# Kernel tuning notes

Hardware: AMD Instinct MI355X
Metric: run time of the kernel (lower is better)

Reference implementation:

```python
import jax, jax.numpy as jnp
import numpy as np

# Static point-cloud layout: B clouds of P points each (batch ids are contiguous equal-size segments)
B, P, C = 16, 4096, 64
RATIO, K = 0.25, 32
S = int(P * RATIO)  # 1024 sampled points per cloud
H1, H2, OUT = 64, 64, 128
CIN = C + 3


def _fps(pos):
    """Farthest point sampling on one cloud. pos: [P,3] -> idx [S] (start at point 0)."""
    Pn = pos.shape[0]
    def step(carry, _):
        dist, far = carry
        d = jnp.sum((pos - pos[far]) ** 2, axis=-1)   # sq dist to newest sample
        dist = jnp.minimum(dist, d)                    # dist to nearest selected point
        nxt = jnp.argmax(dist).astype(jnp.int32)
        return (dist, nxt), far
    init = (jnp.full((Pn,), jnp.inf, pos.dtype), jnp.int32(0))
    _, idx = jax.lax.scan(step, init, None, length=S)
    return idx


def _gather(a, i):
    # a: [B, P, ...], i: [B, ...int] -> per-batch fancy gather
    return jax.vmap(lambda ab, ib: ab[ib])(a, i)


def setup_inputs() -> dict:
    key = jax.random.key(0)
    ks = jax.random.split(key, 6)
    N = B * P
    x = jax.random.normal(ks[0], (N, C), jnp.float32)
    pos = jax.random.uniform(ks[1], (N, 3), jnp.float32)  # points in unit cube
    batch = jnp.repeat(jnp.arange(B, dtype=jnp.int32), P)
    W1 = jax.random.normal(ks[2], (CIN, H1), jnp.float32) / np.float32(np.sqrt(CIN))
    b1 = jnp.zeros((H1,), jnp.float32)
    W2 = jax.random.normal(ks[3], (H1, H2), jnp.float32) / np.float32(np.sqrt(H1))
    b2 = jnp.zeros((H2,), jnp.float32)
    W3 = jax.random.normal(ks[4], (H2, OUT), jnp.float32) / np.float32(np.sqrt(H2))
    b3 = jnp.zeros((OUT,), jnp.float32)
    return {"x": x, "pos": pos, "batch": batch,
            "W1": W1, "b1": b1, "W2": W2, "b2": b2, "W3": W3, "b3": b3}


def reference(x, pos, batch, W1, b1, W2, b2, W3, b3):
    xb = x.reshape(B, P, C)
    pb = pos.reshape(B, P, 3)
    bb = batch.reshape(B, P)

    # 1) FPS sampling per cloud
    idx = jax.vmap(_fps)(pb)                                   # [B,S]
    pos_q = _gather(pb, idx)                                   # [B,S,3]

    # 2) kNN grouping: k nearest original points for each sampled point
    d2 = jnp.sum((pos_q[:, :, None, :] - pb[:, None, :, :]) ** 2, axis=-1)  # [B,S,P]
    _, nbr = jax.lax.top_k(-d2, K)                             # [B,S,K]

    # 3) PointNetConv: MLP(concat[x_j, pos_j - pos_i]) then max-aggregate over neighbors
    x_j = _gather(xb, nbr)                                     # [B,S,K,C]
    p_j = _gather(pb, nbr)                                     # [B,S,K,3]
    rel = p_j - pos_q[:, :, None, :]
    h = jnp.concatenate([x_j, rel], axis=-1)                   # [B,S,K,C+3]
    h = jax.nn.relu(h @ W1 + b1)
    h = jax.nn.relu(h @ W2 + b2)
    h = h @ W3 + b3                                            # plain last layer (PyG MLP plain_last)
    out = jnp.max(h, axis=2)                                   # [B,S,OUT]  max aggr

    batch_q = _gather(bb, idx)                                 # [B,S]
    return out.reshape(B * S, OUT), pos_q.reshape(B * S, 3), batch_q.reshape(B * S)
```

## Files before the change

kernel.cpp:

```cpp
#include <hip/hip_runtime.h>
#include <math.h>
#include <string.h>

#define NB   16
#define NP   4096
#define NC   64
#define NS   1024
#define NK   32
#define NH1  64
#define NH2  64
#define NOUT 128

typedef unsigned long long u64;
typedef unsigned int u32;
typedef unsigned short u16;
typedef __attribute__((ext_vector_type(8))) short s16x8;
typedef __attribute__((ext_vector_type(4))) float f32x4;

__device__ inline u64 umin64(u64 a, u64 b) { return a < b ? a : b; }
__device__ inline u64 umax64(u64 a, u64 b) { return a > b ? a : b; }

__device__ inline u16 f2bf(float f) {
  u32 x = __float_as_uint(f);
  return (u16)((x + 0x7fffu + ((x >> 16) & 1u)) >> 16);
}
__device__ inline u32 pack2bf(float a, float b) {
  return (u32)f2bf(a) | ((u32)f2bf(b) << 16);
}

__device__ inline float d2exact(float ax, float ay, float az,
                                float qx, float qy, float qz) {
  float dx = __fsub_rn(ax, qx), dy = __fsub_rn(ay, qy), dz = __fsub_rn(az, qz);
  return __fadd_rn(__fadd_rn(__fmul_rn(dx, dx), __fmul_rn(dy, dy)),
                   __fmul_rn(dz, dz));
}

#define DPP_LVL_MAX(CTRL)                                                     \
  {                                                                           \
    u32 lo = (u32)key, hi = (u32)(key >> 32);                                 \
    u32 plo = (u32)__builtin_amdgcn_update_dpp((int)lo, (int)lo, CTRL, 0xF, 0xF, false); \
    u32 phi = (u32)__builtin_amdgcn_update_dpp((int)hi, (int)hi, CTRL, 0xF, 0xF, false); \
    u64 ok = ((u64)phi << 32) | plo;                                          \
    key = (ok > key) ? ok : key;                                              \
  }
__device__ inline u64 dpp_wavemax_u64(u64 key) {
  DPP_LVL_MAX(0x111) DPP_LVL_MAX(0x112) DPP_LVL_MAX(0x114)
  DPP_LVL_MAX(0x118) DPP_LVL_MAX(0x142) DPP_LVL_MAX(0x143)
  return key;
}
#define DPP_LVL_MIN(CTRL)                                                     \
  {                                                                           \
    u32 lo = (u32)key, hi = (u32)(key >> 32);                                 \
    u32 plo = (u32)__builtin_amdgcn_update_dpp((int)lo, (int)lo, CTRL, 0xF, 0xF, false); \
    u32 phi = (u32)__builtin_amdgcn_update_dpp((int)hi, (int)hi, CTRL, 0xF, 0xF, false); \
    u64 ok = ((u64)phi << 32) | plo;                                          \
    key = (ok < key) ? ok : key;                                              \
  }
__device__ inline u64 dpp_wavemin_bcast_u64(u64 key) {
  DPP_LVL_MIN(0x111) DPP_LVL_MIN(0x112) DPP_LVL_MIN(0x114)
  DPP_LVL_MIN(0x118) DPP_LVL_MIN(0x142) DPP_LVL_MIN(0x143)
  u32 lo = (u32)__builtin_amdgcn_readlane((int)(u32)key, 63);
  u32 hi = (u32)__builtin_amdgcn_readlane((int)(u32)(key >> 32), 63);
  return ((u64)hi << 32) | lo;
}

#define DPP_FMAX_STAGE(CTRL)                                                  \
  do {                                                                        \
    _Pragma("unroll")                                                         \
    for (int mt = 0; mt < 8; ++mt) {                                          \
      _Pragma("unroll")                                                       \
      for (int r = 0; r < 4; ++r) {                                           \
        int vi = __float_as_int(m[mt][r]);                                    \
        int ov = __builtin_amdgcn_update_dpp(vi, vi, CTRL, 0xF, 0xF, false);  \
        m[mt][r] = fmaxf(m[mt][r], __int_as_float(ov));                       \
      }                                                                       \
    }                                                                         \
  } while (0)

__global__ __launch_bounds__(256) void fps_kernel(const float* __restrict__ pos,
                                                  float* __restrict__ pos_q,
                                                  float* __restrict__ batch_q) {
  const int b = blockIdx.x;
  const int tid = threadIdx.x;
  const int wave = tid >> 6;
  const float* pb = pos + (size_t)b * NP * 3;

  __shared__ float lx[NP], ly[NP], lz[NP];
  __shared__ u64 s_key[2][4];
  __shared__ int s_idx[NS];

  float px[16], py[16], pz[16], dist[16];
#pragma unroll
  for (int i = 0; i < 16; ++i) {
    int p = i * 256 + tid;
    float xx = pb[p * 3 + 0];
    float yy = pb[p * 3 + 1];
    float zz = pb[p * 3 + 2];
    px[i] = xx; py[i] = yy; pz[i] = zz;
    lx[p] = xx; ly[p] = yy; lz[p] = zz;
    dist[i] = __builtin_inff();
  }
  __syncthreads();

  float fx = lx[0], fy = ly[0], fz = lz[0];
  int far = 0;

  for (int s = 0; s < NS; ++s) {
    if (tid == 0) s_idx[s] = far;

    float bv = -1.0f; int bp = 0;
#pragma unroll
    for (int i = 0; i < 16; ++i) {
      float dx = __fsub_rn(px[i], fx);
      float dy = __fsub_rn(py[i], fy);
      float dz = __fsub_rn(pz[i], fz);
      float d = __fadd_rn(__fadd_rn(__fmul_rn(dx, dx), __fmul_rn(dy, dy)),
                          __fmul_rn(dz, dz));
      d = fminf(dist[i], d);
      dist[i] = d;
      if (d > bv) { bv = d; bp = i * 256 + tid; }
    }

    u64 key = ((u64)__float_as_uint(bv) << 32) | (u32)(NP - 1 - bp);
    key = dpp_wavemax_u64(key);
    if ((tid & 63) == 63) s_key[s & 1][wave] = key;
    __syncthreads();

    u64 k0 = s_key[s & 1][0];
    u64 k1 = s_key[s & 1][1];
    u64 k2 = s_key[s & 1][2];
    u64 k3 = s_key[s & 1][3];
    u64 km = umax64(umax64(k0, k1), umax64(k2, k3));
    far = NP - 1 - (int)(u32)(km & 0xFFFFFFFFull);
    fx = lx[far]; fy = ly[far]; fz = lz[far];
  }
  __syncthreads();

  for (int s = tid; s < NS; s += 256) {
    int p = s_idx[s];
    size_t o = (size_t)(b * NS + s);
    pos_q[o * 3 + 0] = lx[p];
    pos_q[o * 3 + 1] = ly[p];
    pos_q[o * 3 + 2] = lz[p];
    batch_q[o] = (float)b;
  }
}

__device__ inline void ins4(u64& b0, u64& b1, u64& b2, u64& b3, u64 k) {
  u64 m0 = umax64(b0, k); b0 = umin64(b0, k);
  u64 m1 = umax64(b1, m0); b1 = umin64(b1, m0);
  u64 m2 = umax64(b2, m1); b2 = umin64(b2, m1);
  b3 = umin64(b3, m2);
}

__global__ __launch_bounds__(64) void knn_kernel(const float* __restrict__ pos,
                                                 const float* __restrict__ pos_q,
                                                 int* __restrict__ nbr) {
  const u64 KMAX = ~0ull;
  const int q = blockIdx.x;
  const int b = q >> 10;
  const int lane = threadIdx.x;
  const float* pb = pos + (size_t)b * NP * 3;
  const float qx = pos_q[q * 3 + 0];
  const float qy = pos_q[q * 3 + 1];
  const float qz = pos_q[q * 3 + 2];

  u64 b0 = KMAX, b1 = KMAX, b2 = KMAX, b3 = KMAX;
#pragma unroll 4
  for (int gg = 0; gg < 16; ++gg) {
    int p = gg * 256 + lane * 4;
    const float* s = pb + (size_t)p * 3;
    float4 v0 = *(const float4*)(s);
    float4 v1 = *(const float4*)(s + 4);
    float4 v2 = *(const float4*)(s + 8);
    float d0 = d2exact(v0.x, v0.y, v0.z, qx, qy, qz);
    float d1 = d2exact(v0.w, v1.x, v1.y, qx, qy, qz);
    float d2 = d2exact(v1.z, v1.w, v2.x, qx, qy, qz);
    float d3 = d2exact(v2.y, v2.z, v2.w, qx, qy, qz);
    ins4(b0, b1, b2, b3, ((u64)__float_as_uint(d0) << 32) | (u32)(p + 0));
    ins4(b0, b1, b2, b3, ((u64)__float_as_uint(d1) << 32) | (u32)(p + 1));
    ins4(b0, b1, b2, b3, ((u64)__float_as_uint(d2) << 32) | (u32)(p + 2));
    ins4(b0, b1, b2, b3, ((u64)__float_as_uint(d3) << 32) | (u32)(p + 3));
  }

  u64 exmask = 0ull;
  for (int r = 0; r < NK; ++r) {
    u64 kmin = dpp_wavemin_bcast_u64(b0);
    u32 p = (u32)kmin;
    if (lane == 0) nbr[q * NK + r] = (int)p;
    if (((p >> 2) & 63u) == (u32)lane) {
      b0 = b1; b1 = b2; b2 = b3; b3 = KMAX;
      exmask |= 1ull << (((p >> 8) << 2) | (p & 3u));
      if (b0 == KMAX) {
        for (int gg = 0; gg < 16; ++gg) {
          int pp = gg * 256 + lane * 4;
          const float* s = pb + (size_t)pp * 3;
          float4 v0 = *(const float4*)(s);
          float4 v1 = *(const float4*)(s + 4);
          float4 v2 = *(const float4*)(s + 8);
          float dd[4];
          dd[0] = d2exact(v0.x, v0.y, v0.z, qx, qy, qz);
          dd[1] = d2exact(v0.w, v1.x, v1.y, qx, qy, qz);
          dd[2] = d2exact(v1.z, v1.w, v2.x, qx, qy, qz);
          dd[3] = d2exact(v2.y, v2.z, v2.w, qx, qy, qz);
#pragma unroll
          for (int rr = 0; rr < 4; ++rr) {
            int slot = gg * 4 + rr;
            if ((exmask >> slot) & 1ull) continue;
            ins4(b0, b1, b2, b3,
                 ((u64)__float_as_uint(dd[rr]) << 32) | (u32)(pp + rr));
          }
        }
      }
    }
  }
}

#define WF_L2 6144
#define WF_L3 10240
#define WF_TOT 18432

__global__ __launch_bounds__(256) void prep_kernel(
    const float* __restrict__ W1, const float* __restrict__ W2,
    const float* __restrict__ W3, u16* __restrict__ wf) {
  int flat = blockIdx.x * 256 + threadIdx.x;
  if (flat >= WF_TOT) return;
  float val;
  int j = flat & 7, lane = (flat >> 3) & 63, t = flat >> 9;
  int k8 = 8 * (lane >> 4) + j, li = lane & 15;
  if (flat < WF_L2) {
    int kc = t % 3, mt = t / 3;
    int k = kc * 32 + k8;
    val = (k < 67) ? W1[k * 64 + mt * 16 + li] : 0.0f;
  } else if (flat < WF_L3) {
    t -= WF_L2 >> 9;
    int kc = t & 1, mt = t >> 1;
    val = W2[(kc * 32 + k8) * 64 + mt * 16 + li];
  } else {
    t -= WF_L3 >> 9;
    int kc = t & 1, mt = t >> 1;
    val = W3[(kc * 32 + k8) * 128 + mt * 16 + li];
  }
  wf[flat] = f2bf(val);
}

#define HST 72

__global__ __launch_bounds__(256) void conv_kernel(
    const float* __restrict__ x, const float* __restrict__ pos,
    const u16* __restrict__ wf,
    const float* __restrict__ b1, const float* __restrict__ b2,
    const float* __restrict__ b3,
    const int* __restrict__ nbr, const float* __restrict__ pos_q,
    float* __restrict__ out) {
  __shared__ u16 Hs[4][32][HST];

  const int tid = threadIdx.x, wave = tid >> 6, lane = tid & 63;
  const int q = blockIdx.x * 4 + wave;
  const int b = q >> 10;
  const int g = lane >> 4, li = lane & 15;

  const int n0 = nbr[q * NK + li];
  const int n1 = nbr[q * NK + li + 16];
  const float qx = pos_q[q * 3 + 0];
  const float qy = pos_q[q * 3 + 1];
  const float qz = pos_q[q * 3 + 2];

  uint4 bf1[2][3];
  {
    const float* xb = x + (size_t)b * NP * NC;
#pragma unroll
    for (int nt = 0; nt < 2; ++nt) {
      const float* s = xb + (size_t)(nt ? n1 : n0) * NC + 8 * g;
#pragma unroll
      for (int kc = 0; kc < 2; ++kc) {
        float4 v0 = *(const float4*)(s + kc * 32);
        float4 v1 = *(const float4*)(s + kc * 32 + 4);
        bf1[nt][kc] = make_uint4(pack2bf(v0.x, v0.y), pack2bf(v0.z, v0.w),
                                 pack2bf(v1.x, v1.y), pack2bf(v1.z, v1.w));
      }
      const float* pp = pos + ((size_t)b * NP + (nt ? n1 : n0)) * 3;
      float rx = __fsub_rn(pp[0], qx);
      float ry = __fsub_rn(pp[1], qy);
      float rz = __fsub_rn(pp[2], qz);
      uint4 w = make_uint4(0u, 0u, 0u, 0u);
      if (g == 0) { w.x = pack2bf(rx, ry); w.y = pack2bf(rz, 0.0f); }
      bf1[nt][2] = w;
    }
  }

  const uint4* wf4 = (const uint4*)wf;

  {
    f32x4 acc[4][2];
#pragma unroll
    for (int mt = 0; mt < 4; ++mt) {
      float4 bb = *(const float4*)(b1 + mt * 16 + 4 * g);
      acc[mt][0] = f32x4{bb.x, bb.y, bb.z, bb.w};
      acc[mt][1] = acc[mt][0];
    }
#pragma unroll
    for (int mt = 0; mt < 4; ++mt)
#pragma unroll
      for (int kc = 0; kc < 3; ++kc) {
        uint4 aw = wf4[(mt * 3 + kc) * 64 + lane];
        s16x8 a = __builtin_bit_cast(s16x8, aw);
        acc[mt][0] = __builtin_amdgcn_mfma_f32_16x16x32_bf16(
            a, __builtin_bit_cast(s16x8, bf1[0][kc]), acc[mt][0], 0, 0, 0);
        acc[mt][1] = __builtin_amdgcn_mfma_f32_16x16x32_bf16(
            a, __builtin_bit_cast(s16x8, bf1[1][kc]), acc[mt][1], 0, 0, 0);
      }
#pragma unroll
    for (int mt = 0; mt < 4; ++mt)
#pragma unroll
      for (int nt = 0; nt < 2; ++nt) {
        f32x4 v = acc[mt][nt];
        u32 w0 = pack2bf(fmaxf(v[0], 0.f), fmaxf(v[1], 0.f));
        u32 w1 = pack2bf(fmaxf(v[2], 0.f), fmaxf(v[3], 0.f));
        *(uint2*)&Hs[wave][li + 16 * nt][mt * 16 + 4 * g] = make_uint2(w0, w1);
      }
  }
  asm volatile("s_waitcnt lgkmcnt(0)" ::: "memory");

  {
    uint4 bf2[2][2];
#pragma unroll
    for (int nt = 0; nt < 2; ++nt)
#pragma unroll
      for (int kc = 0; kc < 2; ++kc)
        bf2[nt][kc] = *(const uint4*)&Hs[wave][li + 16 * nt][kc * 32 + 8 * g];

    f32x4 acc[4][2];
#pragma unroll
    for (int mt = 0; mt < 4; ++mt) {
      float4 bb = *(const float4*)(b2 + mt * 16 + 4 * g);
      acc[mt][0] = f32x4{bb.x, bb.y, bb.z, bb.w};
      acc[mt][1] = acc[mt][0];
    }
#pragma unroll
    for (int mt = 0; mt < 4; ++mt)
#pragma unroll
      for (int kc = 0; kc < 2; ++kc) {
        uint4 aw = wf4[(WF_L2 >> 3) + (mt * 2 + kc) * 64 + lane];
        s16x8 a = __builtin_bit_cast(s16x8, aw);
        acc[mt][0] = __builtin_amdgcn_mfma_f32_16x16x32_bf16(
            a, __builtin_bit_cast(s16x8, bf2[0][kc]), acc[mt][0], 0, 0, 0);
        acc[mt][1] = __builtin_amdgcn_mfma_f32_16x16x32_bf16(
            a, __builtin_bit_cast(s16x8, bf2[1][kc]), acc[mt][1], 0, 0, 0);
      }
#pragma unroll
    for (int mt = 0; mt < 4; ++mt)
#pragma unroll
      for (int nt = 0; nt < 2; ++nt) {
        f32x4 v = acc[mt][nt];
        u32 w0 = pack2bf(fmaxf(v[0], 0.f), fmaxf(v[1], 0.f));
        u32 w1 = pack2bf(fmaxf(v[2], 0.f), fmaxf(v[3], 0.f));
        *(uint2*)&Hs[wave][li + 16 * nt][mt * 16 + 4 * g] = make_uint2(w0, w1);
      }
  }
  asm volatile("s_waitcnt lgkmcnt(0)" ::: "memory");

  {
    uint4 bf3[2][2];
#pragma unroll
    for (int nt = 0; nt < 2; ++nt)
#pragma unroll
      for (int kc = 0; kc < 2; ++kc)
        bf3[nt][kc] = *(const uint4*)&Hs[wave][li + 16 * nt][kc * 32 + 8 * g];

    f32x4 acc[8][2];
#pragma unroll
    for (int mt = 0; mt < 8; ++mt) {
      float4 bb = *(const float4*)(b3 + mt * 16 + 4 * g);
      acc[mt][0] = f32x4{bb.x, bb.y, bb.z, bb.w};
      acc[mt][1] = acc[mt][0];
    }
#pragma unroll
    for (int mt = 0; mt < 8; ++mt)
#pragma unroll
      for (int kc = 0; kc < 2; ++kc) {
        uint4 aw = wf4[(WF_L3 >> 3) + (mt * 2 + kc) * 64 + lane];
        s16x8 a = __builtin_bit_cast(s16x8, aw);
        acc[mt][0] = __builtin_amdgcn_mfma_f32_16x16x32_bf16(
            a, __builtin_bit_cast(s16x8, bf3[0][kc]), acc[mt][0], 0, 0, 0);
        acc[mt][1] = __builtin_amdgcn_mfma_f32_16x16x32_bf16(
            a, __builtin_bit_cast(s16x8, bf3[1][kc]), acc[mt][1], 0, 0, 0);
      }

    float m[8][4];
#pragma unroll
    for (int mt = 0; mt < 8; ++mt)
#pragma unroll
      for (int r = 0; r < 4; ++r)
        m[mt][r] = fmaxf(acc[mt][0][r], acc[mt][1][r]);

    DPP_FMAX_STAGE(0xB1);
    DPP_FMAX_STAGE(0x4E);
    DPP_FMAX_STAGE(0x141);
    DPP_FMAX_STAGE(0x140);

#pragma unroll
    for (int mt = 0; mt < 8; ++mt) {
      if (li == mt) {
        float4 o = make_float4(m[mt][0], m[mt][1], m[mt][2], m[mt][3]);
        *(float4*)(out + (size_t)q * NOUT + mt * 16 + 4 * g) = o;
      }
    }
  }
}

extern "C" void kernel_launch(void* const* d_in, const int* in_sizes, int n_in,
                              void* d_out, int out_size, void* d_ws, size_t ws_size,
                              hipStream_t stream) {
  (void)in_sizes; (void)n_in; (void)out_size; (void)ws_size;
  const float* x   = (const float*)d_in[0];
  const float* pos = (const float*)d_in[1];
  const float* W1 = (const float*)d_in[3];
  const float* b1 = (const float*)d_in[4];
  const float* W2 = (const float*)d_in[5];
  const float* b2 = (const float*)d_in[6];
  const float* W3 = (const float*)d_in[7];
  const float* b3 = (const float*)d_in[8];

  float* out     = (float*)d_out;
  float* pos_q   = out + (size_t)NB * NS * NOUT;
  float* batch_q = pos_q + (size_t)NB * NS * 3;

  int* nbr = (int*)d_ws;
  u16* wfrag = (u16*)((char*)d_ws + (size_t)NB * NS * NK * 4);

  hipLaunchKernelGGL(prep_kernel, dim3((WF_TOT + 255) / 256), dim3(256), 0,
                     stream, W1, W2, W3, wfrag);
  hipLaunchKernelGGL(fps_kernel, dim3(NB), dim3(256), 0, stream,
                     pos, pos_q, batch_q);
  hipLaunchKernelGGL(knn_kernel, dim3(NB * NS), dim3(64), 0, stream,
                     pos, pos_q, nbr);
  hipLaunchKernelGGL(conv_kernel, dim3(NB * NS / 4), dim3(256), 0, stream,
                     x, pos, wfrag, b1, b2, b3, nbr, pos_q, out);
}
```

Before: 781.1 us.

## Fuse FPS, kNN and conv into one cooperative persistent kernel with progress flags

Merges the FPS, kNN and PointNet conv kernels into a single cooperative launch. Sixteen blocks run FPS and publish sampled positions plus a per-cloud progress counter with release stores. The remaining blocks pull query indices from an atomic work queue, spin until their sample is published, then run kNN and the MLP in registers without writing neighbour indices to global memory. This overlaps the serial FPS phase with the kNN/conv work and removes the nbr round-trip and separate launches, at the cost of spin-waiting, a fixed grid of 256 blocks at one block per CU, and dependence on the work queue ordering to avoid deadlock.

New measurement: 1.148 ms. +47.0%, slower.

```diff
diff --git a/kernel.cpp b/kernel.cpp
--- a/kernel.cpp
+++ b/kernel.cpp
@@ -1,15 +1,13 @@
 #include <hip/hip_runtime.h>
 #include <math.h>
-#include <string.h>
 
 #define NB   16
 #define NP   4096
 #define NC   64
 #define NS   1024
 #define NK   32
-#define NH1  64
-#define NH2  64
 #define NOUT 128
+#define NQ   (NB * NS)
 
 typedef unsigned long long u64;
 typedef unsigned int u32;
@@ -77,75 +75,6 @@
     }                                                                         \
   } while (0)
 
-__global__ __launch_bounds__(256) void fps_kernel(const float* __restrict__ pos,
-                                                  float* __restrict__ pos_q,
-                                                  float* __restrict__ batch_q) {
-  const int b = blockIdx.x;
-  const int tid = threadIdx.x;
-  const int wave = tid >> 6;
-  const float* pb = pos + (size_t)b * NP * 3;
-
-  __shared__ float lx[NP], ly[NP], lz[NP];
-  __shared__ u64 s_key[2][4];
-  __shared__ int s_idx[NS];
-
-  float px[16], py[16], pz[16], dist[16];
-#pragma unroll
-  for (int i = 0; i < 16; ++i) {
-    int p = i * 256 + tid;
-    float xx = pb[p * 3 + 0];
-    float yy = pb[p * 3 + 1];
-    float zz = pb[p * 3 + 2];
-    px[i] = xx; py[i] = yy; pz[i] = zz;
-    lx[p] = xx; ly[p] = yy; lz[p] = zz;
-    dist[i] = __builtin_inff();
-  }
-  __syncthreads();
-
-  float fx = lx[0], fy = ly[0], fz = lz[0];
-  int far = 0;
-
-  for (int s = 0; s < NS; ++s) {
-    if (tid == 0) s_idx[s] = far;
-
-    float bv = -1.0f; int bp = 0;
-#pragma unroll
-    for (int i = 0; i < 16; ++i) {
-      float dx = __fsub_rn(px[i], fx);
-      float dy = __fsub_rn(py[i], fy);
-      float dz = __fsub_rn(pz[i], fz);
-      float d = __fadd_rn(__fadd_rn(__fmul_rn(dx, dx), __fmul_rn(dy, dy)),
-                          __fmul_rn(dz, dz));
-      d = fminf(dist[i], d);
-      dist[i] = d;
-      if (d > bv) { bv = d; bp = i * 256 + tid; }
-    }
-
-    u64 key = ((u64)__float_as_uint(bv) << 32) | (u32)(NP - 1 - bp);
-    key = dpp_wavemax_u64(key);
-    if ((tid & 63) == 63) s_key[s & 1][wave] = key;
-    __syncthreads();
-
-    u64 k0 = s_key[s & 1][0];
-    u64 k1 = s_key[s & 1][1];
-    u64 k2 = s_key[s & 1][2];
-    u64 k3 = s_key[s & 1][3];
-    u64 km = umax64(umax64(k0, k1), umax64(k2, k3));
-    far = NP - 1 - (int)(u32)(km & 0xFFFFFFFFull);
-    fx = lx[far]; fy = ly[far]; fz = lz[far];
-  }
-  __syncthreads();
-
-  for (int s = tid; s < NS; s += 256) {
-    int p = s_idx[s];
-    size_t o = (size_t)(b * NS + s);
-    pos_q[o * 3 + 0] = lx[p];
-    pos_q[o * 3 + 1] = ly[p];
-    pos_q[o * 3 + 2] = lz[p];
-    batch_q[o] = (float)b;
-  }
-}
-
 __device__ inline void ins4(u64& b0, u64& b1, u64& b2, u64& b3, u64 k) {
   u64 m0 = umax64(b0, k); b0 = umin64(b0, k);
   u64 m1 = umax64(b1, m0); b1 = umin64(b1, m0);
@@ -153,76 +82,15 @@
   b3 = umin64(b3, m2);
 }
 
-__global__ __launch_bounds__(64) void knn_kernel(const float* __restrict__ pos,
-                                                 const float* __restrict__ pos_q,
-                                                 int* __restrict__ nbr) {
-  const u64 KMAX = ~0ull;
-  const int q = blockIdx.x;
-  const int b = q >> 10;
-  const int lane = threadIdx.x;
-  const float* pb = pos + (size_t)b * NP * 3;
-  const float qx = pos_q[q * 3 + 0];
-  const float qy = pos_q[q * 3 + 1];
-  const float qz = pos_q[q * 3 + 2];
-
-  u64 b0 = KMAX, b1 = KMAX, b2 = KMAX, b3 = KMAX;
-#pragma unroll 4
-  for (int gg = 0; gg < 16; ++gg) {
-    int p = gg * 256 + lane * 4;
-    const float* s = pb + (size_t)p * 3;
-    float4 v0 = *(const float4*)(s);
-    float4 v1 = *(const float4*)(s + 4);
-    float4 v2 = *(const float4*)(s + 8);
-    float d0 = d2exact(v0.x, v0.y, v0.z, qx, qy, qz);
-    float d1 = d2exact(v0.w, v1.x, v1.y, qx, qy, qz);
-    float d2 = d2exact(v1.z, v1.w, v2.x, qx, qy, qz);
-    float d3 = d2exact(v2.y, v2.z, v2.w, qx, qy, qz);
-    ins4(b0, b1, b2, b3, ((u64)__float_as_uint(d0) << 32) | (u32)(p + 0));
-    ins4(b0, b1, b2, b3, ((u64)__float_as_uint(d1) << 32) | (u32)(p + 1));
-    ins4(b0, b1, b2, b3, ((u64)__float_as_uint(d2) << 32) | (u32)(p + 2));
-    ins4(b0, b1, b2, b3, ((u64)__float_as_uint(d3) << 32) | (u32)(p + 3));
-  }
-
-  u64 exmask = 0ull;
-  for (int r = 0; r < NK; ++r) {
-    u64 kmin = dpp_wavemin_bcast_u64(b0);
-    u32 p = (u32)kmin;
-    if (lane == 0) nbr[q * NK + r] = (int)p;
-    if (((p >> 2) & 63u) == (u32)lane) {
-      b0 = b1; b1 = b2; b2 = b3; b3 = KMAX;
-      exmask |= 1ull << (((p >> 8) << 2) | (p & 3u));
-      if (b0 == KMAX) {
-        for (int gg = 0; gg < 16; ++gg) {
-          int pp = gg * 256 + lane * 4;
-          const float* s = pb + (size_t)pp * 3;
-          float4 v0 = *(const float4*)(s);
-          float4 v1 = *(const float4*)(s + 4);
-          float4 v2 = *(const float4*)(s + 8);
-          float dd[4];
-          dd[0] = d2exact(v0.x, v0.y, v0.z, qx, qy, qz);
-          dd[1] = d2exact(v0.w, v1.x, v1.y, qx, qy, qz);
-          dd[2] = d2exact(v1.z, v1.w, v2.x, qx, qy, qz);
-          dd[3] = d2exact(v2.y, v2.z, v2.w, qx, qy, qz);
-#pragma unroll
-          for (int rr = 0; rr < 4; ++rr) {
-            int slot = gg * 4 + rr;
-            if ((exmask >> slot) & 1ull) continue;
-            ins4(b0, b1, b2, b3,
-                 ((u64)__float_as_uint(dd[rr]) << 32) | (u32)(pp + rr));
-          }
-        }
-      }
-    }
-  }
-}
-
 #define WF_L2 6144
 #define WF_L3 10240
 #define WF_TOT 18432
 
 __global__ __launch_bounds__(256) void prep_kernel(
     const float* __restrict__ W1, const float* __restrict__ W2,
-    const float* __restrict__ W3, u16* __restrict__ wf) {
+    const float* __restrict__ W3, u16* __restrict__ wf,
+    u32* __restrict__ ctrl) {
+  if (blockIdx.x == 0 && threadIdx.x < 64) ctrl[threadIdx.x] = 0u;
   int flat = blockIdx.x * 256 + threadIdx.x;
   if (flat >= WF_TOT) return;
   float val;
@@ -246,164 +114,301 @@
 
 #define HST 72
 
-__global__ __launch_bounds__(256) void conv_kernel(
+struct FpsMem { float lx[NP], ly[NP], lz[NP]; u64 s_key[2][4]; };
+struct WMem   { u16 Hs[4][32][HST]; };
+union SMem    { FpsMem f; WMem w; };
+
+__global__ __launch_bounds__(256, 1) void fused_kernel(
     const float* __restrict__ x, const float* __restrict__ pos,
     const u16* __restrict__ wf,
     const float* __restrict__ b1, const float* __restrict__ b2,
     const float* __restrict__ b3,
-    const int* __restrict__ nbr, const float* __restrict__ pos_q,
-    float* __restrict__ out) {
-  __shared__ u16 Hs[4][32][HST];
-
-  const int tid = threadIdx.x, wave = tid >> 6, lane = tid & 63;
-  const int q = blockIdx.x * 4 + wave;
-  const int b = q >> 10;
+    u32* __restrict__ ctrl,
+    float* __restrict__ out, float* __restrict__ pos_q,
+    float* __restrict__ batch_q) {
+  __shared__ SMem sm;
+  const int tid = threadIdx.x;
+  const int wave = tid >> 6, lane = tid & 63;
+  u32* queue = ctrl;
+  u32* prog = ctrl + 32;
+
+  if (blockIdx.x < NB) {
+    const int b = blockIdx.x;
+    const float* pb = pos + (size_t)b * NP * 3;
+
+    float px[16], py[16], pz[16], dist[16];
+#pragma unroll
+    for (int i = 0; i < 16; ++i) {
+      int p = i * 256 + tid;
+      float xx = pb[p * 3 + 0];
+      float yy = pb[p * 3 + 1];
+      float zz = pb[p * 3 + 2];
+      px[i] = xx; py[i] = yy; pz[i] = zz;
+      sm.f.lx[p] = xx; sm.f.ly[p] = yy; sm.f.lz[p] = zz;
+      dist[i] = __builtin_inff();
+    }
+    __syncthreads();
+
+    float fx = sm.f.lx[0], fy = sm.f.ly[0], fz = sm.f.lz[0];
+
+    for (int s = 0; s < NS; ++s) {
+      if (tid == 0) {
+        float* pq = pos_q + (size_t)(b * NS + s) * 3;
+        pq[0] = fx; pq[1] = fy; pq[2] = fz;
+        if ((s & 7) == 7)
+          __hip_atomic_store(&prog[b], (u32)(s + 1), __ATOMIC_RELEASE,
+                             __HIP_MEMORY_SCOPE_AGENT);
+      }
+
+      float bv = -1.0f; int bp = 0;
+#pragma unroll
+      for (int i = 0; i < 16; ++i) {
+        float dx = __fsub_rn(px[i], fx);
+        float dy = __fsub_rn(py[i], fy);
+        float dz = __fsub_rn(pz[i], fz);
+        float d = __fadd_rn(__fadd_rn(__fmul_rn(dx, dx), __fmul_rn(dy, dy)),
+                            __fmul_rn(dz, dz));
+        d = fminf(dist[i], d);
+        dist[i] = d;
+        if (d > bv) { bv = d; bp = i * 256 + tid; }
+      }
+
+      u64 key = ((u64)__float_as_uint(bv) << 32) | (u32)(NP - 1 - bp);
+      key = dpp_wavemax_u64(key);
+      if (lane == 63) sm.f.s_key[s & 1][wave] = key;
+      __syncthreads();
+
+      u64 k0 = sm.f.s_key[s & 1][0];
+      u64 k1 = sm.f.s_key[s & 1][1];
+      u64 k2 = sm.f.s_key[s & 1][2];
+      u64 k3 = sm.f.s_key[s & 1][3];
+      u64 km = umax64(umax64(k0, k1), umax64(k2, k3));
+      int far = NP - 1 - (int)(u32)(km & 0xFFFFFFFFull);
+      fx = sm.f.lx[far]; fy = sm.f.ly[far]; fz = sm.f.lz[far];
+    }
+
+    for (int s = tid; s < NS; s += 256)
+      batch_q[b * NS + s] = (float)b;
+    return;
+  }
+
   const int g = lane >> 4, li = lane & 15;
-
-  const int n0 = nbr[q * NK + li];
-  const int n1 = nbr[q * NK + li + 16];
-  const float qx = pos_q[q * 3 + 0];
-  const float qy = pos_q[q * 3 + 1];
-  const float qz = pos_q[q * 3 + 2];
-
-  uint4 bf1[2][3];
-  {
-    const float* xb = x + (size_t)b * NP * NC;
-#pragma unroll
-    for (int nt = 0; nt < 2; ++nt) {
-      const float* s = xb + (size_t)(nt ? n1 : n0) * NC + 8 * g;
-#pragma unroll
-      for (int kc = 0; kc < 2; ++kc) {
-        float4 v0 = *(const float4*)(s + kc * 32);
-        float4 v1 = *(const float4*)(s + kc * 32 + 4);
-        bf1[nt][kc] = make_uint4(pack2bf(v0.x, v0.y), pack2bf(v0.z, v0.w),
-                                 pack2bf(v1.x, v1.y), pack2bf(v1.z, v1.w));
-      }
-      const float* pp = pos + ((size_t)b * NP + (nt ? n1 : n0)) * 3;
-      float rx = __fsub_rn(pp[0], qx);
-      float ry = __fsub_rn(pp[1], qy);
-      float rz = __fsub_rn(pp[2], qz);
-      uint4 w = make_uint4(0u, 0u, 0u, 0u);
-      if (g == 0) { w.x = pack2bf(rx, ry); w.y = pack2bf(rz, 0.0f); }
-      bf1[nt][2] = w;
-    }
-  }
-
   const uint4* wf4 = (const uint4*)wf;
-
-  {
-    f32x4 acc[4][2];
-#pragma unroll
-    for (int mt = 0; mt < 4; ++mt) {
-      float4 bb = *(const float4*)(b1 + mt * 16 + 4 * g);
-      acc[mt][0] = f32x4{bb.x, bb.y, bb.z, bb.w};
-      acc[mt][1] = acc[mt][0];
-    }
-#pragma unroll
-    for (int mt = 0; mt < 4; ++mt)
-#pragma unroll
-      for (int kc = 0; kc < 3; ++kc) {
-        uint4 aw = wf4[(mt * 3 + kc) * 64 + lane];
-        s16x8 a = __builtin_bit_cast(s16x8, aw);
-        acc[mt][0] = __builtin_amdgcn_mfma_f32_16x16x32_bf16(
-            a, __builtin_bit_cast(s16x8, bf1[0][kc]), acc[mt][0], 0, 0, 0);
-        acc[mt][1] = __builtin_amdgcn_mfma_f32_16x16x32_bf16(
-            a, __builtin_bit_cast(s16x8, bf1[1][kc]), acc[mt][1], 0, 0, 0);
-      }
-#pragma unroll
-    for (int mt = 0; mt < 4; ++mt)
+  const u64 KMAX = ~0ull;
+
+  for (;;) {
+    u32 q;
+    if (lane == 0) q = atomicAdd(queue, 1u);
+    q = (u32)__shfl((int)q, 0, 64);
+    if (q >= (u32)NQ) break;
+    const int b = (int)(q >> 10);
+    const u32 s = q & 1023u;
+
+    while (__hip_atomic_load(&prog[b], __ATOMIC_ACQUIRE,
+                             __HIP_MEMORY_SCOPE_AGENT) <= s)
+      __builtin_amdgcn_s_sleep(32);
+
+    const float* pqf = pos_q + (size_t)q * 3;
+    const float qx = pqf[0];
+    const float qy = pqf[1];
+    const float qz = pqf[2];
+
+    const float* pb = pos + (size_t)b * NP * 3;
+
+    u64 b0 = KMAX, b1k = KMAX, b2k = KMAX, b3k = KMAX;
+#pragma unroll 4
+    for (int gg = 0; gg < 16; ++gg) {
+      int p = gg * 256 + lane * 4;
+      const float* sp = pb + (size_t)p * 3;
+      float4 v0 = *(const float4*)(sp);
+      float4 v1 = *(const float4*)(sp + 4);
+      float4 v2 = *(const float4*)(sp + 8);
+      float d0 = d2exact(v0.x, v0.y, v0.z, qx, qy, qz);
+      float d1 = d2exact(v0.w, v1.x, v1.y, qx, qy, qz);
+      float d2 = d2exact(v1.z, v1.w, v2.x, qx, qy, qz);
+      float d3 = d2exact(v2.y, v2.z, v2.w, qx, qy, qz);
+      ins4(b0, b1k, b2k, b3k, ((u64)__float_as_uint(d0) << 32) | (u32)(p + 0));
+      ins4(b0, b1k, b2k, b3k, ((u64)__float_as_uint(d1) << 32) | (u32)(p + 1));
+      ins4(b0, b1k, b2k, b3k, ((u64)__float_as_uint(d2) << 32) | (u32)(p + 2));
+      ins4(b0, b1k, b2k, b3k, ((u64)__float_as_uint(d3) << 32) | (u32)(p + 3));
+    }
+
+    int n0 = 0, n1 = 0;
+    u64 exmask = 0ull;
+    for (int r = 0; r < NK; ++r) {
+      u64 kmin = dpp_wavemin_bcast_u64(b0);
+      u32 p = (u32)kmin;
+      if (r == li) n0 = (int)p;
+      if (r == li + 16) n1 = (int)p;
+      if (((p >> 2) & 63u) == (u32)lane) {
+        b0 = b1k; b1k = b2k; b2k = b3k; b3k = KMAX;
+        exmask |= 1ull << (((p >> 8) << 2) | (p & 3u));
+        if (b0 == KMAX) {
+          for (int gg = 0; gg < 16; ++gg) {
+            int pp = gg * 256 + lane * 4;
+            const float* sp = pb + (size_t)pp * 3;
+            float4 v0 = *(const float4*)(sp);
+            float4 v1 = *(const float4*)(sp + 4);
+            float4 v2 = *(const float4*)(sp + 8);
+            float dd[4];
+            dd[0] = d2exact(v0.x, v0.y, v0.z, qx, qy, qz);
+            dd[1] = d2exact(v0.w, v1.x, v1.y, qx, qy, qz);
+            dd[2] = d2exact(v1.z, v1.w, v2.x, qx, qy, qz);
+            dd[3] = d2exact(v2.y, v2.z, v2.w, qx, qy, qz);
+#pragma unroll
+            for (int rr = 0; rr < 4; ++rr) {
+              int slot = gg * 4 + rr;
+              if ((exmask >> slot) & 1ull) continue;
+              ins4(b0, b1k, b2k, b3k,
+                   ((u64)__float_as_uint(dd[rr]) << 32) | (u32)(pp + rr));
+            }
+          }
+        }
+      }
+    }
+
+    uint4 bf1[2][3];
+    {
+      const float* xb = x + (size_t)b * NP * NC;
 #pragma unroll
       for (int nt = 0; nt < 2; ++nt) {
-        f32x4 v = acc[mt][nt];
-        u32 w0 = pack2bf(fmaxf(v[0], 0.f), fmaxf(v[1], 0.f));
-        u32 w1 = pack2bf(fmaxf(v[2], 0.f), fmaxf(v[3], 0.f));
-        *(uint2*)&Hs[wave][li + 16 * nt][mt * 16 + 4 * g] = make_uint2(w0, w1);
-      }
-  }
-  asm volatile("s_waitcnt lgkmcnt(0)" ::: "memory");
-
-  {
-    uint4 bf2[2][2];
-#pragma unroll
-    for (int nt = 0; nt < 2; ++nt)
-#pragma unroll
-      for (int kc = 0; kc < 2; ++kc)
-        bf2[nt][kc] = *(const uint4*)&Hs[wave][li + 16 * nt][kc * 32 + 8 * g];
-
-    f32x4 acc[4][2];
-#pragma unroll
-    for (int mt = 0; mt < 4; ++mt) {
-      float4 bb = *(const float4*)(b2 + mt * 16 + 4 * g);
-      acc[mt][0] = f32x4{bb.x, bb.y, bb.z, bb.w};
-      acc[mt][1] = acc[mt][0];
-    }
-#pragma unroll
-    for (int mt = 0; mt < 4; ++mt)
-#pragma unroll
-      for (int kc = 0; kc < 2; ++kc) {
-        uint4 aw = wf4[(WF_L2 >> 3) + (mt * 2 + kc) * 64 + lane];
-        s16x8 a = __builtin_bit_cast(s16x8, aw);
-        acc[mt][0] = __builtin_amdgcn_mfma_f32_16x16x32_bf16(
-            a, __builtin_bit_cast(s16x8, bf2[0][kc]), acc[mt][0], 0, 0, 0);
-        acc[mt][1] = __builtin_amdgcn_mfma_f32_16x16x32_bf16(
-            a, __builtin_bit_cast(s16x8, bf2[1][kc]), acc[mt][1], 0, 0, 0);
-      }
-#pragma unroll
-    for (int mt = 0; mt < 4; ++mt)
-#pragma unroll
-      for (int nt = 0; nt < 2; ++nt) {
-        f32x4 v = acc[mt][nt];
-        u32 w0 = pack2bf(fmaxf(v[0], 0.f), fmaxf(v[1], 0.f));
-        u32 w1 = pack2bf(fmaxf(v[2], 0.f), fmaxf(v[3], 0.f));
-        *(uint2*)&Hs[wave][li + 16 * nt][mt * 16 + 4 * g] = make_uint2(w0, w1);
-      }
-  }
-  asm volatile("s_waitcnt lgkmcnt(0)" ::: "memory");
-
-  {
-    uint4 bf3[2][2];
-#pragma unroll
-    for (int nt = 0; nt < 2; ++nt)
-#pragma unroll
-      for (int kc = 0; kc < 2; ++kc)
-        bf3[nt][kc] = *(const uint4*)&Hs[wave][li + 16 * nt][kc * 32 + 8 * g];
-
-    f32x4 acc[8][2];
-#pragma unroll
-    for (int mt = 0; mt < 8; ++mt) {
-      float4 bb = *(const float4*)(b3 + mt * 16 + 4 * g);
-      acc[mt][0] = f32x4{bb.x, bb.y, bb.z, bb.w};
-      acc[mt][1] = acc[mt][0];
-    }
-#pragma unroll
-    for (int mt = 0; mt < 8; ++mt)
-#pragma unroll
-      for (int kc = 0; kc < 2; ++kc) {
-        uint4 aw = wf4[(WF_L3 >> 3) + (mt * 2 + kc) * 64 + lane];
-        s16x8 a = __builtin_bit_cast(s16x8, aw);
-        acc[mt][0] = __builtin_amdgcn_mfma_f32_16x16x32_bf16(
-            a, __builtin_bit_cast(s16x8, bf3[0][kc]), acc[mt][0], 0, 0, 0);
-        acc[mt][1] = __builtin_amdgcn_mfma_f32_16x16x32_bf16(
-            a, __builtin_bit_cast(s16x8, bf3[1][kc]), acc[mt][1], 0, 0, 0);
-      }
-
-    float m[8][4];
-#pragma unroll
-    for (int mt = 0; mt < 8; ++mt)
-#pragma unroll
-      for (int r = 0; r < 4; ++r)
-        m[mt][r] = fmaxf(acc[mt][0][r], acc[mt][1][r]);
-
-    DPP_FMAX_STAGE(0xB1);
-    DPP_FMAX_STAGE(0x4E);
-    DPP_FMAX_STAGE(0x141);
-    DPP_FMAX_STAGE(0x140);
-
-#pragma unroll
-    for (int mt = 0; mt < 8; ++mt) {
-      if (li == mt) {
-        float4 o = make_float4(m[mt][0], m[mt][1], m[mt][2], m[mt][3]);
-        *(float4*)(out + (size_t)q * NOUT + mt * 16 + 4 * g) = o;
+        const float* sp = xb + (size_t)(nt ? n1 : n0) * NC + 8 * g;
+#pragma unroll
+        for (int kc = 0; kc < 2; ++kc) {
+          float4 v0 = *(const float4*)(sp + kc * 32);
+          float4 v1 = *(const float4*)(sp + kc * 32 + 4);
+          bf1[nt][kc] = make_uint4(pack2bf(v0.x, v0.y), pack2bf(v0.z, v0.w),
+                                   pack2bf(v1.x, v1.y), pack2bf(v1.z, v1.w));
+        }
+        const float* pp = pos + ((size_t)b * NP + (nt ? n1 : n0)) * 3;
+        float rx = __fsub_rn(pp[0], qx);
+        float ry = __fsub_rn(pp[1], qy);
+        float rz = __fsub_rn(pp[2], qz);
+        uint4 w = make_uint4(0u, 0u, 0u, 0u);
+        if (g == 0) { w.x = pack2bf(rx, ry); w.y = pack2bf(rz, 0.0f); }
+        bf1[nt][2] = w;
+      }
+    }
+
+    {
+      f32x4 acc[4][2];
+#pragma unroll
+      for (int mt = 0; mt < 4; ++mt) {
+        float4 bb = *(const float4*)(b1 + mt * 16 + 4 * g);
+        acc[mt][0] = f32x4{bb.x, bb.y, bb.z, bb.w};
+        acc[mt][1] = acc[mt][0];
+      }
+#pragma unroll
+      for (int mt = 0; mt < 4; ++mt)
+#pragma unroll
+        for (int kc = 0; kc < 3; ++kc) {
+          uint4 aw = wf4[(mt * 3 + kc) * 64 + lane];
+          s16x8 a = __builtin_bit_cast(s16x8, aw);
+          acc[mt][0] = __builtin_amdgcn_mfma_f32_16x16x32_bf16(
+              a, __builtin_bit_cast(s16x8, bf1[0][kc]), acc[mt][0], 0, 0, 0);
+          acc[mt][1] = __builtin_amdgcn_mfma_f32_16x16x32_bf16(
+              a, __builtin_bit_cast(s16x8, bf1[1][kc]), acc[mt][1], 0, 0, 0);
+        }
+#pragma unroll
+      for (int mt = 0; mt < 4; ++mt)
+#pragma unroll
+        for (int nt = 0; nt < 2; ++nt) {
+          f32x4 v = acc[mt][nt];
+          u32 w0 = pack2bf(fmaxf(v[0], 0.f), fmaxf(v[1], 0.f));
+          u32 w1 = pack2bf(fmaxf(v[2], 0.f), fmaxf(v[3], 0.f));
+          *(uint2*)&sm.w.Hs[wave][li + 16 * nt][mt * 16 + 4 * g] =
+              make_uint2(w0, w1);
+        }
+    }
+    asm volatile("s_waitcnt lgkmcnt(0)" ::: "memory");
+
+    {
+      uint4 bf2[2][2];
+#pragma unroll
+      for (int nt = 0; nt < 2; ++nt)
+#pragma unroll
+        for (int kc = 0; kc < 2; ++kc)
+          bf2[nt][kc] =
+              *(const uint4*)&sm.w.Hs[wave][li + 16 * nt][kc * 32 + 8 * g];
+
+      f32x4 acc[4][2];
+#pragma unroll
+      for (int mt = 0; mt < 4; ++mt) {
+        float4 bb = *(const float4*)(b2 + mt * 16 + 4 * g);
+        acc[mt][0] = f32x4{bb.x, bb.y, bb.z, bb.w};
+        acc[mt][1] = acc[mt][0];
+      }
+#pragma unroll
+      for (int mt = 0; mt < 4; ++mt)
+#pragma unroll
+        for (int kc = 0; kc < 2; ++kc) {
+          uint4 aw = wf4[(WF_L2 >> 3) + (mt * 2 + kc) * 64 + lane];
+          s16x8 a = __builtin_bit_cast(s16x8, aw);
+          acc[mt][0] = __builtin_amdgcn_mfma_f32_16x16x32_bf16(
+              a, __builtin_bit_cast(s16x8, bf2[0][kc]), acc[mt][0], 0, 0, 0);
+          acc[mt][1] = __builtin_amdgcn_mfma_f32_16x16x32_bf16(
+              a, __builtin_bit_cast(s16x8, bf2[1][kc]), acc[mt][1], 0, 0, 0);
+        }
+      asm volatile("s_waitcnt lgkmcnt(0)" ::: "memory");
+#pragma unroll
+      for (int mt = 0; mt < 4; ++mt)
+#pragma unroll
+        for (int nt = 0; nt < 2; ++nt) {
+          f32x4 v = acc[mt][nt];
+          u32 w0 = pack2bf(fmaxf(v[0], 0.f), fmaxf(v[1], 0.f));
+          u32 w1 = pack2bf(fmaxf(v[2], 0.f), fmaxf(v[3], 0.f));
+          *(uint2*)&sm.w.Hs[wave][li + 16 * nt][mt * 16 + 4 * g] =
+              make_uint2(w0, w1);
+        }
+    }
+    asm volatile("s_waitcnt lgkmcnt(0)" ::: "memory");
+
+    {
+      uint4 bf3[2][2];
+#pragma unroll
+      for (int nt = 0; nt < 2; ++nt)
+#pragma unroll
+        for (int kc = 0; kc < 2; ++kc)
+          bf3[nt][kc] =
+              *(const uint4*)&sm.w.Hs[wave][li + 16 * nt][kc * 32 + 8 * g];
+
+      f32x4 acc[8][2];
+#pragma unroll
+      for (int mt = 0; mt < 8; ++mt) {
+        float4 bb = *(const float4*)(b3 + mt * 16 + 4 * g);
+        acc[mt][0] = f32x4{bb.x, bb.y, bb.z, bb.w};
+        acc[mt][1] = acc[mt][0];
+      }
+#pragma unroll
+      for (int mt = 0; mt < 8; ++mt)
+#pragma unroll
+        for (int kc = 0; kc < 2; ++kc) {
+          uint4 aw = wf4[(WF_L3 >> 3) + (mt * 2 + kc) * 64 + lane];
+          s16x8 a = __builtin_bit_cast(s16x8, aw);
+          acc[mt][0] = __builtin_amdgcn_mfma_f32_16x16x32_bf16(
+              a, __builtin_bit_cast(s16x8, bf3[0][kc]), acc[mt][0], 0, 0, 0);
+          acc[mt][1] = __builtin_amdgcn_mfma_f32_16x16x32_bf16(
+              a, __builtin_bit_cast(s16x8, bf3[1][kc]), acc[mt][1], 0, 0, 0);
+        }
+
+      float m[8][4];
+#pragma unroll
+      for (int mt = 0; mt < 8; ++mt)
+#pragma unroll
+        for (int r = 0; r < 4; ++r)
+          m[mt][r] = fmaxf(acc[mt][0][r], acc[mt][1][r]);
+
+      DPP_FMAX_STAGE(0xB1);
+      DPP_FMAX_STAGE(0x4E);
+      DPP_FMAX_STAGE(0x141);
+      DPP_FMAX_STAGE(0x140);
+
+#pragma unroll
+      for (int mt = 0; mt < 8; ++mt) {
+        if (li == mt) {
+          float4 o = make_float4(m[mt][0], m[mt][1], m[mt][2], m[mt][3]);
+          *(float4*)(out + (size_t)q * NOUT + mt * 16 + 4 * g) = o;
+        }
       }
     }
   }
@@ -426,15 +431,15 @@
   float* pos_q   = out + (size_t)NB * NS * NOUT;
   float* batch_q = pos_q + (size_t)NB * NS * 3;
 
-  int* nbr = (int*)d_ws;
-  u16* wfrag = (u16*)((char*)d_ws + (size_t)NB * NS * NK * 4);
+  u32* ctrl = (u32*)d_ws;
+  u16* wfrag = (u16*)((char*)d_ws + 256);
 
   hipLaunchKernelGGL(prep_kernel, dim3((WF_TOT + 255) / 256), dim3(256), 0,
-                     stream, W1, W2, W3, wfrag);
-  hipLaunchKernelGGL(fps_kernel, dim3(NB), dim3(256), 0, stream,
-                     pos, pos_q, batch_q);
-  hipLaunchKernelGGL(knn_kernel, dim3(NB * NS), dim3(64), 0, stream,
-                     pos, pos_q, nbr);
-  hipLaunchKernelGGL(conv_kernel, dim3(NB * NS / 4), dim3(256), 0, stream,
-                     x, pos, wfrag, b1, b2, b3, nbr, pos_q, out);
-}
+                     stream, W1, W2, W3, wfrag, ctrl);
+
+  void* args[] = {(void*)&x,  (void*)&pos, (void*)&wfrag, (void*)&b1,
+                  (void*)&b2, (void*)&b3,  (void*)&ctrl,  (void*)&out,
+                  (void*)&pos_q, (void*)&batch_q};
+  hipLaunchCooperativeKernel((const void*)fused_kernel, dim3(256), dim3(256),
+                             args, 0, stream);
+}
```
